# Kernel optimization log

Measured on AMD Instinct MI355X. Metric: run time of the kernel, lower is better.

## Reference

```python
import jax, jax.numpy as jnp
import numpy as np

WS = 11      # window_size
SIGMA = 1.5
C1 = 0.01 ** 2
C2 = 0.03 ** 2


def _window(channel):
    g = np.exp(-((np.arange(WS) - WS // 2) ** 2) / (2.0 * SIGMA ** 2))
    g = (g / g.sum()).astype(np.float32)
    w2 = np.outer(g, g)  # [WS, WS]
    return jnp.asarray(np.broadcast_to(w2, (channel, 1, WS, WS)).copy())


def _blur(x, w, channel):
    pad = WS // 2
    return jax.lax.conv_general_dilated(
        x, w, window_strides=(1, 1), padding=[(pad, pad), (pad, pad)],
        dimension_numbers=("NCHW", "OIHW", "NCHW"),
        feature_group_count=channel)


def _ssim(img1, img2, w, channel):
    mu1 = _blur(img1, w, channel)
    mu2 = _blur(img2, w, channel)
    mu1_sq = mu1 * mu1
    mu2_sq = mu2 * mu2
    mu1_mu2 = mu1 * mu2
    sigma1_sq = _blur(img1 * img1, w, channel) - mu1_sq
    sigma2_sq = _blur(img2 * img2, w, channel) - mu2_sq
    sigma12 = _blur(img1 * img2, w, channel) - mu1_mu2
    ssim_map = ((2.0 * mu1_mu2 + C1) * (2.0 * sigma12 + C2)) / (
        (mu1_sq + mu2_sq + C1) * (sigma1_sq + sigma2_sq + C2))
    return ssim_map.mean()  # size_average=True


def setup_inputs() -> dict:
    key = jax.random.key(0)
    k1, k2, k3 = jax.random.split(key, 3)
    B, C, H, W = 16, 3, 512, 512
    return {
        "fused_img": jax.random.uniform(k1, (B, C, H, W), dtype=jnp.float32),
        "source_img1": jax.random.uniform(k2, (B, C, H, W), dtype=jnp.float32),
        "source_img2": jax.random.uniform(k3, (B, C, H, W), dtype=jnp.float32),
    }


def reference(fused_img, source_img1, source_img2):
    channel = fused_img.shape[1]
    w = _window(channel).astype(fused_img.dtype)
    ssim1 = _ssim(fused_img, source_img1, w, channel)
    ssim2 = _ssim(fused_img, source_img2, w, channel)
    return 1.0 - (ssim1 + ssim2) / 2.0
```

## Files before the change

### kernel.cpp

```cpp
#include <hip/hip_runtime.h>
#include <cmath>

#define HALO 5
#define TSX 32
#define TILE_H 128
#define NCHUNK 4
#define CH 32
#define RING 42
#define HSTR 36
#define PLANE (RING * HSTR)
#define WIDTH 512
#define HEIGHT 512

struct GW { float g[11]; };

__device__ __forceinline__ float ssim2(float mu1, float mu2,
                                       float x2b, float y2b, float xyb)
{
    const float C1 = 1e-4f, C2 = 9e-4f;
    float mu12 = mu1 * mu2;
    float num  = (2.f * mu12 + C1) * (2.f * (xyb - mu12) + C2);
    float den  = (mu1 * mu1 + mu2 * mu2 + C1) *
                 ((x2b - mu1 * mu1) + (y2b - mu2 * mu2) + C2);
    return num * __builtin_amdgcn_rcpf(den);
}

template<bool CX, bool CY>
__device__ __forceinline__ float tile_compute(
    const float* __restrict__ fI, const float* __restrict__ aI,
    const float* __restrict__ bI, float (* __restrict__ hb)[PLANE],
    const GW& gw, int tid, int x0, int y0, size_t pbase)
{
    const int rA  = tid >> 3;
    const int qA  = tid & 7;
    const int gx0 = x0 + 4 * qA - 8;
    const int jB  = tid & 31;
    const int rgB = tid >> 5;

    float part = 0.f;

    #pragma unroll 1
    for (int c = 0; c < NCHUNK; ++c) {
        if (c) __syncthreads();

        const int nA = c ? CH : RING;
        #pragma unroll 1
        for (int t0 = rA; t0 < nA; t0 += 32) {
            const int t = c ? (CH * c + 2 * HALO + t0) : t0;
            int slot = t;
            slot -= (slot >= RING) ? RING : 0;
            slot -= (slot >= RING) ? RING : 0;
            slot -= (slot >= RING) ? RING : 0;
            const int yy = y0 - HALO + t;
            const bool yok = CY ? ((unsigned)yy < (unsigned)HEIGHT) : true;
            const float* rowf = fI + pbase + (size_t)yy * WIDTH;
            const float* rowa = aI + pbase + (size_t)yy * WIDTH;
            const float* rowb = bI + pbase + (size_t)yy * WIDTH;

            float acc[4][8];
            #pragma unroll
            for (int jj = 0; jj < 4; ++jj)
                #pragma unroll
                for (int q = 0; q < 8; ++q) acc[jj][q] = 0.f;

            if (yok) {
                #pragma unroll
                for (int k = 0; k < 5; ++k) {
                    const int g = gx0 + 4 * k;
                    float4 vf, va, vb;
                    if (CX) {
                        const bool ok = ((unsigned)g <= (unsigned)(WIDTH - 4));
                        vf = ok ? *(const float4*)(rowf + g) : make_float4(0,0,0,0);
                        va = ok ? *(const float4*)(rowa + g) : make_float4(0,0,0,0);
                        vb = ok ? *(const float4*)(rowb + g) : make_float4(0,0,0,0);
                    } else {
                        vf = *(const float4*)(rowf + g);
                        va = *(const float4*)(rowa + g);
                        vb = *(const float4*)(rowb + g);
                    }
                    const float fs[4] = { vf.x, vf.y, vf.z, vf.w };
                    const float as[4] = { va.x, va.y, va.z, va.w };
                    const float bs[4] = { vb.x, vb.y, vb.z, vb.w };
                    #pragma unroll
                    for (int cc = 0; cc < 4; ++cc) {
                        const int tt = 4 * k + cc - 3;
                        if (tt < 0 || tt > 13) continue;
                        const float f = fs[cc], a = as[cc], b = bs[cc];
                        float p[8];
                        p[0] = f; p[1] = a; p[2] = b;
                        p[3] = f * f; p[4] = a * a; p[5] = b * b;
                        p[6] = f * a; p[7] = f * b;
                        #pragma unroll
                        for (int jj = 0; jj < 4; ++jj) {
                            const int u = tt - jj;
                            if (u >= 0 && u <= 10) {
                                const float w = gw.g[u];
                                #pragma unroll
                                for (int q = 0; q < 8; ++q)
                                    acc[jj][q] = fmaf(w, p[q], acc[jj][q]);
                            }
                        }
                    }
                }
            }
            #pragma unroll
            for (int q = 0; q < 8; ++q)
                *(float4*)(&hb[q][slot * HSTR + 4 * qA]) =
                    make_float4(acc[0][q], acc[1][q], acc[2][q], acc[3][q]);
        }
        __syncthreads();

        int sb = CH * c + 4 * rgB;
        sb -= (sb >= RING) ? RING : 0;
        sb -= (sb >= RING) ? RING : 0;
        float acc2[4][8];
        #pragma unroll
        for (int ri = 0; ri < 4; ++ri)
            #pragma unroll
            for (int q = 0; q < 8; ++q) acc2[ri][q] = 0.f;
        #pragma unroll
        for (int k = 0; k < 14; ++k) {
            int s = sb + k;
            s -= (s >= RING) ? RING : 0;
            const float* hp = &hb[0][s * HSTR + jB];
            float hv[8];
            #pragma unroll
            for (int q = 0; q < 8; ++q) hv[q] = hp[q * PLANE];
            #pragma unroll
            for (int ri = 0; ri < 4; ++ri) {
                const int u = k - ri;
                if (u >= 0 && u <= 10) {
                    const float w = gw.g[u];
                    #pragma unroll
                    for (int q = 0; q < 8; ++q)
                        acc2[ri][q] = fmaf(w, hv[q], acc2[ri][q]);
                }
            }
        }
        #pragma unroll
        for (int ri = 0; ri < 4; ++ri) {
            part += ssim2(acc2[ri][0], acc2[ri][1],
                          acc2[ri][3], acc2[ri][4], acc2[ri][6]);
            part += ssim2(acc2[ri][0], acc2[ri][2],
                          acc2[ri][3], acc2[ri][5], acc2[ri][7]);
        }
    }
    return part;
}

__global__ __launch_bounds__(256, 3)
void ssim_tile(const float* __restrict__ fI, const float* __restrict__ aI,
               const float* __restrict__ bI, float* __restrict__ bsum,
               GW gw)
{
    __shared__ __align__(16) float hb[8][PLANE];
    __shared__ float red[4];

    const int tid = threadIdx.x;
    const int x0 = blockIdx.x * TSX;
    const int y0 = blockIdx.y * TILE_H;
    const size_t pbase = (size_t)blockIdx.z * (size_t)(WIDTH * HEIGHT);

    const bool ex = (blockIdx.x == 0) || (blockIdx.x == gridDim.x - 1);
    const bool ey = (blockIdx.y == 0) || (blockIdx.y == gridDim.y - 1);

    float part;
    if (!ex && !ey)
        part = tile_compute<false, false>(fI, aI, bI, hb, gw, tid, x0, y0, pbase);
    else if (!ex)
        part = tile_compute<false, true >(fI, aI, bI, hb, gw, tid, x0, y0, pbase);
    else if (!ey)
        part = tile_compute<true,  false>(fI, aI, bI, hb, gw, tid, x0, y0, pbase);
    else
        part = tile_compute<true,  true >(fI, aI, bI, hb, gw, tid, x0, y0, pbase);

    #pragma unroll
    for (int off = 32; off > 0; off >>= 1) part += __shfl_down(part, off);
    if ((tid & 63) == 0) red[tid >> 6] = part;
    __syncthreads();
    if (tid == 0) {
        int bid = blockIdx.x + gridDim.x * (blockIdx.y + gridDim.y * blockIdx.z);
        bsum[bid] = red[0] + red[1] + red[2] + red[3];
    }
}

__global__ __launch_bounds__(256)
void ssim_final(const float* __restrict__ bsum, float* __restrict__ out,
                int nb, float invTwoN)
{
    __shared__ float sred[4];
    float s = 0.f;
    for (int i = threadIdx.x; i < nb; i += 256) s += bsum[i];
    #pragma unroll
    for (int off = 32; off > 0; off >>= 1) s += __shfl_down(s, off);
    if ((threadIdx.x & 63) == 0) sred[threadIdx.x >> 6] = s;
    __syncthreads();
    if (threadIdx.x == 0)
        out[0] = 1.f - (sred[0] + sred[1] + sred[2] + sred[3]) * invTwoN;
}

extern "C" void kernel_launch(void* const* d_in, const int* in_sizes, int n_in,
                              void* d_out, int out_size, void* d_ws, size_t ws_size,
                              hipStream_t stream)
{
    const float* f  = (const float*)d_in[0];
    const float* s1 = (const float*)d_in[1];
    const float* s2 = (const float*)d_in[2];
    float* out  = (float*)d_out;
    float* bsum = (float*)d_ws;

    const int N = in_sizes[0];
    const int planes = N / (WIDTH * HEIGHT);

    GW gw;
    double gd[11], gs = 0.0;
    for (int i = 0; i < 11; ++i) {
        double d = (double)(i - 5);
        gd[i] = exp(-(d * d) / 4.5);
        gs += gd[i];
    }
    for (int i = 0; i < 11; ++i) gw.g[i] = (float)(gd[i] / gs);

    dim3 grid(WIDTH / TSX, HEIGHT / TILE_H, planes);
    const int nb = (WIDTH / TSX) * (HEIGHT / TILE_H) * planes;
    ssim_tile<<<grid, dim3(256), 0, stream>>>(f, s1, s2, bsum, gw);
    ssim_final<<<1, dim3(256), 0, stream>>>(bsum, out, nb, 0.5f / (float)N);
}
```

Measured before the change: 265.6 us.

## Warp-specialize tile into concurrent horizontal and vertical blur groups

Splits the 256-thread block into two halves: the first 128 threads horizontally blur the next 16 rows into the shared ring buffer while the other 128 vertically blur and compute SSIM for the current 16-row chunk. The goal is to overlap global loads and horizontal-pass work with vertical-pass work, using one barrier per step instead of two phases separated by barriers. In exchange there are twice as many steps and barriers, each half does half the block's work, and the two halves' workloads may not be balanced.

```diff
diff --git a/kernel.cpp b/kernel.cpp
--- a/kernel.cpp
+++ b/kernel.cpp
@@ -4,8 +4,8 @@
 #define HALO 5
 #define TSX 32
 #define TILE_H 128
-#define NCHUNK 4
-#define CH 32
+#define NSTEP 8
+#define CH 16
 #define RING 42
 #define HSTR 36
 #define PLANE (RING * HSTR)
@@ -26,6 +26,64 @@
 }
 
 template<bool CX, bool CY>
+__device__ __forceinline__ void hblur_row(
+    const float* __restrict__ rowf, const float* __restrict__ rowa,
+    const float* __restrict__ rowb, bool yok, int gx0, int slot, int qA,
+    float (* __restrict__ hb)[PLANE], const GW& gw)
+{
+    float acc[4][8];
+    #pragma unroll
+    for (int jj = 0; jj < 4; ++jj)
+        #pragma unroll
+        for (int q = 0; q < 8; ++q) acc[jj][q] = 0.f;
+
+    #pragma unroll
+    for (int k = 0; k < 5; ++k) {
+        const int g = gx0 + 4 * k;
+        float4 vf, va, vb;
+        if (CX || CY) {
+            bool ok = true;
+            if (CY) ok = yok;
+            if (CX) ok = ok && ((unsigned)g <= (unsigned)(WIDTH - 4));
+            vf = ok ? *(const float4*)(rowf + g) : make_float4(0,0,0,0);
+            va = ok ? *(const float4*)(rowa + g) : make_float4(0,0,0,0);
+            vb = ok ? *(const float4*)(rowb + g) : make_float4(0,0,0,0);
+        } else {
+            vf = *(const float4*)(rowf + g);
+            va = *(const float4*)(rowa + g);
+            vb = *(const float4*)(rowb + g);
+        }
+        const float fs[4] = { vf.x, vf.y, vf.z, vf.w };
+        const float as[4] = { va.x, va.y, va.z, va.w };
+        const float bs[4] = { vb.x, vb.y, vb.z, vb.w };
+        #pragma unroll
+        for (int cc = 0; cc < 4; ++cc) {
+            const int tt = 4 * k + cc - 3;
+            if (tt < 0 || tt > 13) continue;
+            const float f = fs[cc], a = as[cc], b = bs[cc];
+            float p[8];
+            p[0] = f; p[1] = a; p[2] = b;
+            p[3] = f * f; p[4] = a * a; p[5] = b * b;
+            p[6] = f * a; p[7] = f * b;
+            #pragma unroll
+            for (int jj = 0; jj < 4; ++jj) {
+                const int u = tt - jj;
+                if (u >= 0 && u <= 10) {
+                    const float w = gw.g[u];
+                    #pragma unroll
+                    for (int q = 0; q < 8; ++q)
+                        acc[jj][q] = fmaf(w, p[q], acc[jj][q]);
+                }
+            }
+        }
+    }
+    #pragma unroll
+    for (int q = 0; q < 8; ++q)
+        *(float4*)(&hb[q][slot * HSTR + 4 * qA]) =
+            make_float4(acc[0][q], acc[1][q], acc[2][q], acc[3][q]);
+}
+
+template<bool CX, bool CY>
 __device__ __forceinline__ float tile_compute(
     const float* __restrict__ fI, const float* __restrict__ aI,
     const float* __restrict__ bI, float (* __restrict__ hb)[PLANE],
@@ -35,115 +93,73 @@
     const int qA  = tid & 7;
     const int gx0 = x0 + 4 * qA - 8;
     const int jB  = tid & 31;
-    const int rgB = tid >> 5;
+    const int rgB = (tid >> 5) & 3;
 
     float part = 0.f;
 
+    if (rA < 26) {
+        const int yy = y0 - HALO + rA;
+        const bool yok = CY ? ((unsigned)yy < (unsigned)HEIGHT) : true;
+        hblur_row<CX, CY>(fI + pbase + (size_t)yy * WIDTH,
+                          aI + pbase + (size_t)yy * WIDTH,
+                          bI + pbase + (size_t)yy * WIDTH,
+                          yok, gx0, rA, qA, hb, gw);
+    }
+    __syncthreads();
+
     #pragma unroll 1
-    for (int c = 0; c < NCHUNK; ++c) {
-        if (c) __syncthreads();
-
-        const int nA = c ? CH : RING;
-        #pragma unroll 1
-        for (int t0 = rA; t0 < nA; t0 += 32) {
-            const int t = c ? (CH * c + 2 * HALO + t0) : t0;
-            int slot = t;
-            slot -= (slot >= RING) ? RING : 0;
-            slot -= (slot >= RING) ? RING : 0;
-            slot -= (slot >= RING) ? RING : 0;
-            const int yy = y0 - HALO + t;
-            const bool yok = CY ? ((unsigned)yy < (unsigned)HEIGHT) : true;
-            const float* rowf = fI + pbase + (size_t)yy * WIDTH;
-            const float* rowa = aI + pbase + (size_t)yy * WIDTH;
-            const float* rowb = bI + pbase + (size_t)yy * WIDTH;
-
-            float acc[4][8];
-            #pragma unroll
-            for (int jj = 0; jj < 4; ++jj)
+    for (int s = 0; s < NSTEP; ++s) {
+        if (tid < 128) {
+            if (s < NSTEP - 1) {
+                const int t = CH * s + RING - CH + rA;
+                int slot = t;
+                slot -= (slot >= RING) ? RING : 0;
+                slot -= (slot >= RING) ? RING : 0;
+                slot -= (slot >= RING) ? RING : 0;
+                const int yy = y0 - HALO + t;
+                const bool yok = CY ? ((unsigned)yy < (unsigned)HEIGHT) : true;
+                hblur_row<CX, CY>(fI + pbase + (size_t)yy * WIDTH,
+                                  aI + pbase + (size_t)yy * WIDTH,
+                                  bI + pbase + (size_t)yy * WIDTH,
+                                  yok, gx0, slot, qA, hb, gw);
+            }
+        } else {
+            int sb = CH * s + 4 * rgB;
+            sb -= (sb >= RING) ? RING : 0;
+            sb -= (sb >= RING) ? RING : 0;
+            float acc2[4][8];
+            #pragma unroll
+            for (int ri = 0; ri < 4; ++ri)
                 #pragma unroll
-                for (int q = 0; q < 8; ++q) acc[jj][q] = 0.f;
-
-            if (yok) {
+                for (int q = 0; q < 8; ++q) acc2[ri][q] = 0.f;
+            #pragma unroll
+            for (int k = 0; k < 14; ++k) {
+                int t = sb + k;
+                t -= (t >= RING) ? RING : 0;
+                const float* hp = &hb[0][t * HSTR + jB];
+                float hv[8];
                 #pragma unroll
-                for (int k = 0; k < 5; ++k) {
-                    const int g = gx0 + 4 * k;
-                    float4 vf, va, vb;
-                    if (CX) {
-                        const bool ok = ((unsigned)g <= (unsigned)(WIDTH - 4));
-                        vf = ok ? *(const float4*)(rowf + g) : make_float4(0,0,0,0);
-                        va = ok ? *(const float4*)(rowa + g) : make_float4(0,0,0,0);
-                        vb = ok ? *(const float4*)(rowb + g) : make_float4(0,0,0,0);
-                    } else {
-                        vf = *(const float4*)(rowf + g);
-                        va = *(const float4*)(rowa + g);
-                        vb = *(const float4*)(rowb + g);
-                    }
-                    const float fs[4] = { vf.x, vf.y, vf.z, vf.w };
-                    const float as[4] = { va.x, va.y, va.z, va.w };
-                    const float bs[4] = { vb.x, vb.y, vb.z, vb.w };
-                    #pragma unroll
-                    for (int cc = 0; cc < 4; ++cc) {
-                        const int tt = 4 * k + cc - 3;
-                        if (tt < 0 || tt > 13) continue;
-                        const float f = fs[cc], a = as[cc], b = bs[cc];
-                        float p[8];
-                        p[0] = f; p[1] = a; p[2] = b;
-                        p[3] = f * f; p[4] = a * a; p[5] = b * b;
-                        p[6] = f * a; p[7] = f * b;
+                for (int q = 0; q < 8; ++q) hv[q] = hp[q * PLANE];
+                #pragma unroll
+                for (int ri = 0; ri < 4; ++ri) {
+                    const int u = k - ri;
+                    if (u >= 0 && u <= 10) {
+                        const float w = gw.g[u];
                         #pragma unroll
-                        for (int jj = 0; jj < 4; ++jj) {
-                            const int u = tt - jj;
-                            if (u >= 0 && u <= 10) {
-                                const float w = gw.g[u];
-                                #pragma unroll
-                                for (int q = 0; q < 8; ++q)
-                                    acc[jj][q] = fmaf(w, p[q], acc[jj][q]);
-                            }
-                        }
+                        for (int q = 0; q < 8; ++q)
+                            acc2[ri][q] = fmaf(w, hv[q], acc2[ri][q]);
                     }
                 }
             }
             #pragma unroll
-            for (int q = 0; q < 8; ++q)
-                *(float4*)(&hb[q][slot * HSTR + 4 * qA]) =
-                    make_float4(acc[0][q], acc[1][q], acc[2][q], acc[3][q]);
+            for (int ri = 0; ri < 4; ++ri) {
+                part += ssim2(acc2[ri][0], acc2[ri][1],
+                              acc2[ri][3], acc2[ri][4], acc2[ri][6]);
+                part += ssim2(acc2[ri][0], acc2[ri][2],
+                              acc2[ri][3], acc2[ri][5], acc2[ri][7]);
+            }
         }
         __syncthreads();
-
-        int sb = CH * c + 4 * rgB;
-        sb -= (sb >= RING) ? RING : 0;
-        sb -= (sb >= RING) ? RING : 0;
-        float acc2[4][8];
-        #pragma unroll
-        for (int ri = 0; ri < 4; ++ri)
-            #pragma unroll
-            for (int q = 0; q < 8; ++q) acc2[ri][q] = 0.f;
-        #pragma unroll
-        for (int k = 0; k < 14; ++k) {
-            int s = sb + k;
-            s -= (s >= RING) ? RING : 0;
-            const float* hp = &hb[0][s * HSTR + jB];
-            float hv[8];
-            #pragma unroll
-            for (int q = 0; q < 8; ++q) hv[q] = hp[q * PLANE];
-            #pragma unroll
-            for (int ri = 0; ri < 4; ++ri) {
-                const int u = k - ri;
-                if (u >= 0 && u <= 10) {
-                    const float w = gw.g[u];
-                    #pragma unroll
-                    for (int q = 0; q < 8; ++q)
-                        acc2[ri][q] = fmaf(w, hv[q], acc2[ri][q]);
-                }
-            }
-        }
-        #pragma unroll
-        for (int ri = 0; ri < 4; ++ri) {
-            part += ssim2(acc2[ri][0], acc2[ri][1],
-                          acc2[ri][3], acc2[ri][4], acc2[ri][6]);
-            part += ssim2(acc2[ri][0], acc2[ri][2],
-                          acc2[ri][3], acc2[ri][5], acc2[ri][7]);
-        }
     }
     return part;
 }
```

New measurement: 255.9 us. -3.7%, faster.
